# Kernel tuning notes

Hardware: AMD Instinct MI355X
Metric: run time of the kernel (lower is better)

The kernel has to match this reference:

```python
import jax, jax.numpy as jnp
import numpy as np

N_NODES = 20000
N_EDGES = 320000
HIDDEN = 128
HEADS = 8
LAYERS = 3
EXP_DEG = 4
N_VIRT = 1
NV = N_NODES + N_VIRT  # nodes after VirtualNode transform


def _layer_norm(x, g, b, eps=1e-5):
    mu = jnp.mean(x, axis=-1, keepdims=True)
    var = jnp.var(x, axis=-1, keepdims=True)
    return (x - mu) * jax.lax.rsqrt(var + eps) * g + b


def _segment_softmax(scores, seg, num_segments):
    # numerically-stable softmax over edges grouped by destination node
    m = jax.ops.segment_max(scores, seg, num_segments=num_segments)
    m = jnp.where(jnp.isfinite(m), m, 0.0)
    e = jnp.exp(scores - m[seg])
    s = jax.ops.segment_sum(e, seg, num_segments=num_segments)
    return e / (s[seg] + 1e-16)


def _edge_attention(x, src, dst, wq, bq, wk, bk, wv, bv, wo, bo):
    # multi-head attention restricted to the given edge list (Exphormer local/expander attention)
    n, d_model = x.shape
    dh = d_model // HEADS
    q = (x @ wq + bq).reshape(n, HEADS, dh)
    k = (x @ wk + bk).reshape(n, HEADS, dh)
    v = (x @ wv + bv).reshape(n, HEADS, dh)
    scores = jnp.einsum('ehd,ehd->eh', q[dst], k[src]) * (1.0 / np.sqrt(dh))  # [E, H]
    alpha = _segment_softmax(scores, dst, n)
    out = jax.ops.segment_sum(alpha[:, :, None] * v[src], dst, num_segments=n)  # [n, H, dh]
    return out.reshape(n, d_model) @ wo + bo


def setup_inputs():
    key = jax.random.key(0)
    ks = jax.random.split(key, 32)
    x = jax.random.normal(ks[0], (N_NODES, HIDDEN), dtype=jnp.float32)
    edge_index = jax.random.randint(ks[1], (2, N_EDGES), 0, N_NODES, dtype=jnp.int32)
    # expander graph per layer: EXP_DEG//2 random permutations, both directions
    ar = jnp.arange(NV, dtype=jnp.int32)
    layers_e = []
    for l in range(LAYERS):
        e = []
        for p in range(EXP_DEG // 2):
            perm = jax.random.permutation(jax.random.fold_in(ks[2], l * 10 + p), NV).astype(jnp.int32)
            e.append(jnp.stack([ar, perm]))
            e.append(jnp.stack([perm, ar]))
        layers_e.append(jnp.concatenate(e, axis=1))
    expander_edges = jnp.stack(layers_e)  # [LAYERS, 2, NV*EXP_DEG]

    def w(k, shape):
        return jax.random.normal(k, shape, dtype=jnp.float32) * 0.05

    p = {}
    names = ['lq', 'lk', 'lv', 'lo', 'eq', 'ek', 'ev', 'eo']
    for i, nm in enumerate(names):
        p[nm + '_w'] = w(ks[3 + i], (LAYERS, HIDDEN, HIDDEN))
        p[nm + '_b'] = w(ks[12 + i], (LAYERS, HIDDEN))
    p['ln_g'] = jnp.ones((LAYERS, HIDDEN), jnp.float32)
    p['ln_b'] = jnp.zeros((LAYERS, HIDDEN), jnp.float32)
    p['ffn_w1'] = w(ks[21], (LAYERS, HIDDEN, 4 * HIDDEN))
    p['ffn_b1'] = w(ks[22], (LAYERS, 4 * HIDDEN))
    p['ffn_w2'] = w(ks[23], (LAYERS, 4 * HIDDEN, HIDDEN))
    p['ffn_b2'] = w(ks[24], (LAYERS, HIDDEN))
    return {'x': x, 'edge_index': edge_index, 'expander_edges': expander_edges, **p}


def reference(x, edge_index, expander_edges,
              lq_w, lq_b, lk_w, lk_b, lv_w, lv_b, lo_w, lo_b,
              eq_w, eq_b, ek_w, ek_b, ev_w, ev_b, eo_w, eo_b,
              ln_g, ln_b, ffn_w1, ffn_b1, ffn_w2, ffn_b2):
    n = x.shape[0]
    # VirtualNode transform: one zero-feature node connected bidirectionally to all nodes
    xv = jnp.concatenate([x, jnp.zeros((N_VIRT, x.shape[1]), x.dtype)], axis=0)
    ar = jnp.arange(n, dtype=edge_index.dtype)
    vn = jnp.full((n,), n, dtype=edge_index.dtype)
    vsrc = jnp.concatenate([edge_index[0], ar, vn])
    vdst = jnp.concatenate([edge_index[1], vn, ar])
    for l in range(LAYERS):
        residual = xv
        local = _edge_attention(xv, vsrc, vdst,
                                lq_w[l], lq_b[l], lk_w[l], lk_b[l],
                                lv_w[l], lv_b[l], lo_w[l], lo_b[l])
        exp_out = _edge_attention(xv, expander_edges[l, 0], expander_edges[l, 1],
                                  eq_w[l], eq_b[l], ek_w[l], ek_b[l],
                                  ev_w[l], ev_b[l], eo_w[l], eo_b[l])
        xv = _layer_norm(residual + local + exp_out, ln_g[l], ln_b[l])
        xv = xv + (jax.nn.gelu(xv @ ffn_w1[l] + ffn_b1[l], approximate=False) @ ffn_w2[l] + ffn_b2[l])
    return xv[:N_NODES]
```

## Files before the change

### kernel.cpp

```cpp
#include <hip/hip_runtime.h>
#include <hip/hip_bf16.h>
#include <math.h>

#define NN    20000
#define NVT   20001
#define VN    20000
#define E_EI  320000
#define E_LOC 360000
#define E_EXP 80004
#define RSN   20002
#define NBVN  79
#define VNSTR 144

#define OW_LQ 0
#define OB_LQ 16384
#define OW_LK 16512
#define OB_LK 32896
#define OW_LV 33024
#define OB_LV 49408
#define OW_LO 49536
#define OB_LO 65920
#define OW_EQ 66048
#define OB_EQ 82432
#define OW_EK 82560
#define OB_EK 98944
#define OW_EV 99072
#define OB_EV 115456
#define OW_EO 115584
#define OB_EO 131968
#define O_LNG 132096
#define O_LNB 132224
#define O_FW1 132352
#define O_FB1 197888
#define O_FW2 198400
#define O_FB2 263936
#define WC_TOT 264064

typedef unsigned short u16;
typedef unsigned int   u32;
typedef __attribute__((ext_vector_type(8))) short short8;
typedef __attribute__((ext_vector_type(4))) float f32x4;

__device__ __forceinline__ float bf2f(u16 u) {
    return __uint_as_float(((u32)u) << 16);
}
__device__ __forceinline__ u16 f2bf(float f) {
    u32 x = __float_as_uint(f);
    u32 r = x + 0x7fffu + ((x >> 16) & 1u);
    return (u16)(r >> 16);
}

__device__ __forceinline__ void loadq16(const u16* qp, float* qf) {
    const uint4* p = (const uint4*)qp;
    uint4 a = p[0], b = p[1];
    qf[0]=bf2f((u16)(a.x&0xffff)); qf[1]=bf2f((u16)(a.x>>16));
    qf[2]=bf2f((u16)(a.y&0xffff)); qf[3]=bf2f((u16)(a.y>>16));
    qf[4]=bf2f((u16)(a.z&0xffff)); qf[5]=bf2f((u16)(a.z>>16));
    qf[6]=bf2f((u16)(a.w&0xffff)); qf[7]=bf2f((u16)(a.w>>16));
    qf[8]=bf2f((u16)(b.x&0xffff)); qf[9]=bf2f((u16)(b.x>>16));
    qf[10]=bf2f((u16)(b.y&0xffff)); qf[11]=bf2f((u16)(b.y>>16));
    qf[12]=bf2f((u16)(b.z&0xffff)); qf[13]=bf2f((u16)(b.z>>16));
    qf[14]=bf2f((u16)(b.w&0xffff)); qf[15]=bf2f((u16)(b.w>>16));
}
__device__ __forceinline__ float dot16_pre(const u16* kp, const float* qf) {
    const uint4* p = (const uint4*)kp;
    uint4 a = p[0], b = p[1];
    float s = 0.f;
    s += qf[0]*bf2f((u16)(a.x&0xffff)) + qf[1]*bf2f((u16)(a.x>>16));
    s += qf[2]*bf2f((u16)(a.y&0xffff)) + qf[3]*bf2f((u16)(a.y>>16));
    s += qf[4]*bf2f((u16)(a.z&0xffff)) + qf[5]*bf2f((u16)(a.z>>16));
    s += qf[6]*bf2f((u16)(a.w&0xffff)) + qf[7]*bf2f((u16)(a.w>>16));
    s += qf[8]*bf2f((u16)(b.x&0xffff)) + qf[9]*bf2f((u16)(b.x>>16));
    s += qf[10]*bf2f((u16)(b.y&0xffff)) + qf[11]*bf2f((u16)(b.y>>16));
    s += qf[12]*bf2f((u16)(b.z&0xffff)) + qf[13]*bf2f((u16)(b.z>>16));
    s += qf[14]*bf2f((u16)(b.w&0xffff)) + qf[15]*bf2f((u16)(b.w>>16));
    return s;
}
__device__ __forceinline__ float dot16_bf(const u16* kptr, const float* qptr) {
    const uint4* kp = (const uint4*)kptr;
    uint4 a = kp[0], b = kp[1];
    const float4* qp = (const float4*)qptr;
    float4 q0 = qp[0], q1 = qp[1], q2 = qp[2], q3 = qp[3];
    float s = 0.f;
    s += q0.x * bf2f((u16)(a.x & 0xffff)) + q0.y * bf2f((u16)(a.x >> 16));
    s += q0.z * bf2f((u16)(a.y & 0xffff)) + q0.w * bf2f((u16)(a.y >> 16));
    s += q1.x * bf2f((u16)(a.z & 0xffff)) + q1.y * bf2f((u16)(a.z >> 16));
    s += q1.z * bf2f((u16)(a.w & 0xffff)) + q1.w * bf2f((u16)(a.w >> 16));
    s += q2.x * bf2f((u16)(b.x & 0xffff)) + q2.y * bf2f((u16)(b.x >> 16));
    s += q2.z * bf2f((u16)(b.y & 0xffff)) + q2.w * bf2f((u16)(b.y >> 16));
    s += q3.x * bf2f((u16)(b.z & 0xffff)) + q3.y * bf2f((u16)(b.z >> 16));
    s += q3.z * bf2f((u16)(b.w & 0xffff)) + q3.w * bf2f((u16)(b.w >> 16));
    return s;
}

__global__ void k_detect(const u16* __restrict__ x, int* __restrict__ flag) {
    int t = threadIdx.x;
    u16 v = x[2 * t];
    int e = (v >> 7) & 0xFF;
    int sane = (e >= 100 && e <= 150) ? 1 : 0;
    __shared__ int s;
    if (t == 0) s = 0;
    __syncthreads();
    atomicAdd(&s, sane);
    __syncthreads();
    if (t == 0) *flag = (s >= 192) ? 1 : 0;
}

__global__ void k_convert(const void* __restrict__ x, const int* __restrict__ flag,
                          u16* __restrict__ XV, int* __restrict__ RS) {
    int i = blockIdx.x * 256 + threadIdx.x;
    if (i < NVT * 128) {
        u16 v = 0;
        if (i < NN * 128)
            v = (*flag) ? ((const u16*)x)[i] : f2bf(((const float*)x)[i]);
        XV[i] = v;
    } else {
        int j = i - NVT * 128;
        if (j < RSN + 4) RS[j] = 0;
    }
}

__global__ void k_canon(
    const void* lqw, const void* lqb, const void* lkw, const void* lkb,
    const void* lvw, const void* lvb, const void* low_, const void* lob,
    const void* eqw, const void* eqb, const void* ekw, const void* ekb,
    const void* evw, const void* evb, const void* eow, const void* eob,
    const void* lng, const void* lnb, const void* f1w, const void* f1b,
    const void* f2w, const void* f2b,
    const int* __restrict__ flag, u16* __restrict__ WcAll)
{
    int idx = blockIdx.x * 256 + threadIdx.x;
    if (idx >= WC_TOT) return;
    int layer = blockIdx.y;
    u16* Wc = WcAll + (size_t)layer * WC_TOT;
    const void* src;
    int e, stride;
    if (idx < 132096) {
        int p = idx / 16512, w = idx - p * 16512;
        const void* wt; const void* bt;
        switch (p) {
            case 0: wt = lqw; bt = lqb; break;
            case 1: wt = lkw; bt = lkb; break;
            case 2: wt = lvw; bt = lvb; break;
            case 3: wt = low_; bt = lob; break;
            case 4: wt = eqw; bt = eqb; break;
            case 5: wt = ekw; bt = ekb; break;
            case 6: wt = evw; bt = evb; break;
            default: wt = eow; bt = eob; break;
        }
        if (w < 16384) {
            int kt = w >> 12, ct = (w >> 9) & 7, ln = (w >> 3) & 63, j = w & 7;
            int k = kt * 32 + (ln >> 4) * 8 + j, c = ct * 16 + (ln & 15);
            src = wt; e = k * 128 + c; stride = 16384;
        } else { src = bt; e = w - 16384; stride = 128; }
    } else {
        int t2 = idx - 132096;
        if (t2 < 128)        { src = lng; e = t2;       stride = 128; }
        else if (t2 < 256)   { src = lnb; e = t2 - 128; stride = 128; }
        else if (t2 < 256 + 65536) {
            int w = t2 - 256;
            int cb = w >> 14, w2 = w & 16383;
            int kt = w2 >> 12, ct = (w2 >> 9) & 7, ln = (w2 >> 3) & 63, j = w2 & 7;
            int k = kt * 32 + (ln >> 4) * 8 + j, c = cb * 128 + ct * 16 + (ln & 15);
            src = f1w; e = k * 512 + c; stride = 65536;
        }
        else if (t2 < 66304) { src = f1b; e = t2 - 65792; stride = 512; }
        else if (t2 < 131840) {
            int w = t2 - 66304;
            int kt = w >> 12, ct = (w >> 9) & 7, ln = (w >> 3) & 63, j = w & 7;
            int k = kt * 32 + (ln >> 4) * 8 + j, c = ct * 16 + (ln & 15);
            src = f2w; e = k * 128 + c; stride = 65536;
        }
        else { src = f2b; e = t2 - 131840; stride = 128; }
    }
    int eg = layer * stride + e;
    Wc[idx] = (*flag) ? ((const u16*)src)[eg] : f2bf(((const float*)src)[eg]);
}

__global__ void k_count(const int* __restrict__ ei, int* __restrict__ RS) {
    int g = blockIdx.x * 256 + threadIdx.x;
    if (g >= E_EI) return;
    atomicAdd(&RS[ei[E_EI + g] + 1], 1);
}

__global__ __launch_bounds__(256) void k_scan(int* __restrict__ RS, int* __restrict__ CUR) {
    int t = threadIdx.x;
    const int CH = 79;
    int base = t * CH;
    int sum = 0;
    for (int i = 0; i < CH; ++i) {
        int idx = base + i;
        if (idx < RSN) {
            int add = RS[idx];
            if (idx >= 1 && idx <= NN) add += 1;
            if (idx == RSN - 1)        add += NN;
            sum += add;
        }
    }
    __shared__ int ss[256];
    ss[t] = sum;
    __syncthreads();
    for (int off = 1; off < 256; off <<= 1) {
        int v = (t >= off) ? ss[t - off] : 0;
        __syncthreads();
        ss[t] += v;
        __syncthreads();
    }
    int run = ss[t] - sum;
    for (int i = 0; i < CH; ++i) {
        int idx = base + i;
        if (idx < RSN) {
            int add = RS[idx];
            if (idx >= 1 && idx <= NN) add += 1;
            if (idx == RSN - 1)        add += NN;
            run += add;
            RS[idx]  = run;
            if (idx < NN) CUR[idx] = run + 1;
        }
    }
}

__global__ void k_scatter(const int* __restrict__ ei, int* __restrict__ CUR,
                          int* __restrict__ CSRC) {
    int g = blockIdx.x * 256 + threadIdx.x;
    if (g >= E_EI) return;
    int src = ei[g], dst = ei[E_EI + g];
    int pos = atomicAdd(&CUR[dst], 1);
    CSRC[pos] = src;
}

__global__ void k_fixinv(const int* __restrict__ RS, int* __restrict__ CSRC,
                         const int* __restrict__ ex, int* __restrict__ IP) {
    int idx = blockIdx.x * 256 + threadIdx.x;
    if (idx < NN) {
        CSRC[RS[idx]] = VN;
        CSRC[RS[VN] + idx] = idx;
    }
    if (idx < 6 * NVT) {
        int p = idx / NVT, i = idx - p * NVT;
        int l = p >> 1, w = p & 1;
        int off = l * 2 * E_EXP + E_EXP + w * 2 * NVT;
        int val = ex[off + i];
        IP[p * NVT + val] = i;
    }
}


__global__ __launch_bounds__(256) void k_qkv(
    const u16* __restrict__ X, const u16* __restrict__ Wc,
    u16* O0, u16* O1, u16* O2)
{
    int z = blockIdx.z;
    int wo = (z == 0) ? OW_LQ : (z == 1) ? OW_LK : OW_LV;
    int bo = (z == 0) ? OB_LQ : (z == 1) ? OB_LK : OB_LV;
    u16* O = (z == 0) ? O0 : (z == 1) ? O1 : O2;
    int t = threadIdx.x;
    int wv = t >> 6, lane = t & 63;
    int q4 = lane >> 4, m = lane & 15;
    int rowb = blockIdx.x * 64 + wv * 16;
    int r0 = min(rowb + m, NVT - 1);
    f32x4 zero4 = {0.f, 0.f, 0.f, 0.f};
    f32x4 acc[8];
    #pragma unroll
    for (int ct = 0; ct < 8; ++ct) acc[ct] = zero4;

    const u16* Wf = Wc + wo + lane * 8;
    #pragma unroll
    for (int kt = 0; kt < 4; ++kt) {
        short8 a0 = *(const short8*)&X[r0 * 128 + kt * 32 + q4 * 8];
        #pragma unroll
        for (int ct = 0; ct < 8; ++ct) {
            short8 bw = *(const short8*)&Wf[kt * 4096 + ct * 512];
            acc[ct] = __builtin_amdgcn_mfma_f32_16x16x32_bf16(bw, a0, acc[ct], 0, 0, 0);
        }
    }
    int row = rowb + m;
    if (row < NVT) {
        #pragma unroll
        for (int ct = 0; ct < 8; ++ct) {
            int c0 = ct * 16 + q4 * 4;
            ushort4 bb = *(const ushort4*)&Wc[bo + c0];
            ushort4 st;
            st.x = f2bf(acc[ct][0] + bf2f(bb.x));
            st.y = f2bf(acc[ct][1] + bf2f(bb.y));
            st.z = f2bf(acc[ct][2] + bf2f(bb.z));
            st.w = f2bf(acc[ct][3] + bf2f(bb.w));
            *(ushort4*)&O[row * 128 + c0] = st;
        }
    }
}

__global__ __launch_bounds__(256) void k_pq(
    u16* ATT, const u16* XV, const u16* __restrict__ Wc,
    u16* Q, u16* K, u16* V)
{
    int z = blockIdx.z;
    const u16* X; u16* O; const u16* A = nullptr;
    int wo, bo;
    if (z == 0)      { X = ATT; O = ATT; A = XV; wo = OW_LO; bo = OB_LO; }
    else if (z == 1) { X = XV;  O = Q;  wo = OW_EQ; bo = OB_EQ; }
    else if (z == 2) { X = XV;  O = K;  wo = OW_EK; bo = OB_EK; }
    else             { X = XV;  O = V;  wo = OW_EV; bo = OB_EV; }

    int t = threadIdx.x;
    int wv = t >> 6, lane = t & 63;
    int q4 = lane >> 4, m = lane & 15;
    int rowb = blockIdx.x * 64 + wv * 16;
    int r0 = min(rowb + m, NVT - 1);
    f32x4 zero4 = {0.f, 0.f, 0.f, 0.f};
    f32x4 acc[8];
    #pragma unroll
    for (int ct = 0; ct < 8; ++ct) acc[ct] = zero4;

    const u16* Wf = Wc + wo + lane * 8;
    #pragma unroll
    for (int kt = 0; kt < 4; ++kt) {
        short8 a0 = *(const short8*)&X[r0 * 128 + kt * 32 + q4 * 8];
        #pragma unroll
        for (int ct = 0; ct < 8; ++ct) {
            short8 bw = *(const short8*)&Wf[kt * 4096 + ct * 512];
            acc[ct] = __builtin_amdgcn_mfma_f32_16x16x32_bf16(bw, a0, acc[ct], 0, 0, 0);
        }
    }
    int row = rowb + m;
    if (row < NVT) {
        #pragma unroll
        for (int ct = 0; ct < 8; ++ct) {
            int c0 = ct * 16 + q4 * 4;
            ushort4 bb = *(const ushort4*)&Wc[bo + c0];
            float v0 = acc[ct][0] + bf2f(bb.x);
            float v1 = acc[ct][1] + bf2f(bb.y);
            float v2 = acc[ct][2] + bf2f(bb.z);
            float v3 = acc[ct][3] + bf2f(bb.w);
            if (A) {
                ushort4 av = *(const ushort4*)&A[row * 128 + c0];
                v0 += bf2f(av.x); v1 += bf2f(av.y);
                v2 += bf2f(av.z); v3 += bf2f(av.w);
            }
            ushort4 st;
            st.x = f2bf(v0); st.y = f2bf(v1); st.z = f2bf(v2); st.w = f2bf(v3);
            *(ushort4*)&O[row * 128 + c0] = st;
        }
    }
}

__global__ __launch_bounds__(256) void k_plf(
    u16* XV, const u16* __restrict__ ATT, const u16* __restrict__ Wc,
    const int* __restrict__ flag, void* outp, int write_out)
{
    __shared__ __align__(16) u16 Xs[32 * 136];
    __shared__ __align__(16) u16 Hs[32 * 520];
    int t = threadIdx.x;
    int wv = t >> 6, lane = t & 63;
    int q4 = lane >> 4, m = lane & 15;
    int rowb = blockIdx.x * 32;
    f32x4 zero4 = {0.f, 0.f, 0.f, 0.f};

    if (wv < 2) {
        int rl = wv * 16 + m;
        int r0 = min(rowb + rl, NVT - 1);
        f32x4 acc[8];
        #pragma unroll
        for (int ct = 0; ct < 8; ++ct) acc[ct] = zero4;
        const u16* Wf = Wc + OW_EO + lane * 8;
        #pragma unroll
        for (int kt = 0; kt < 4; ++kt) {
            short8 a0 = *(const short8*)&XV[r0 * 128 + kt * 32 + q4 * 8];
            #pragma unroll
            for (int ct = 0; ct < 8; ++ct) {
                short8 bw = *(const short8*)&Wf[kt * 4096 + ct * 512];
                acc[ct] = __builtin_amdgcn_mfma_f32_16x16x32_bf16(bw, a0, acc[ct], 0, 0, 0);
            }
        }
        float sm = 0.f, sq = 0.f;
        #pragma unroll
        for (int ct = 0; ct < 8; ++ct) {
            int c0 = ct * 16 + q4 * 4;
            ushort4 bb = *(const ushort4*)&Wc[OB_EO + c0];
            ushort4 av = *(const ushort4*)&ATT[r0 * 128 + c0];
            acc[ct][0] += bf2f(bb.x) + bf2f(av.x);
            acc[ct][1] += bf2f(bb.y) + bf2f(av.y);
            acc[ct][2] += bf2f(bb.z) + bf2f(av.z);
            acc[ct][3] += bf2f(bb.w) + bf2f(av.w);
            #pragma unroll
            for (int j = 0; j < 4; ++j) { sm += acc[ct][j]; sq += acc[ct][j] * acc[ct][j]; }
        }
        sm += __shfl_xor(sm, 16); sq += __shfl_xor(sq, 16);
        sm += __shfl_xor(sm, 32); sq += __shfl_xor(sq, 32);
        float mu  = sm * (1.f / 128.f);
        float var = sq * (1.f / 128.f) - mu * mu;
        float rs  = rsqrtf(var + 1e-5f);
        #pragma unroll
        for (int ct = 0; ct < 8; ++ct) {
            int c0 = ct * 16 + q4 * 4;
            ushort4 gg = *(const ushort4*)&Wc[O_LNG + c0];
            ushort4 bb = *(const ushort4*)&Wc[O_LNB + c0];
            ushort4 st;
            st.x = f2bf((acc[ct][0] - mu) * rs * bf2f(gg.x) + bf2f(bb.x));
            st.y = f2bf((acc[ct][1] - mu) * rs * bf2f(gg.y) + bf2f(bb.y));
            st.z = f2bf((acc[ct][2] - mu) * rs * bf2f(gg.z) + bf2f(bb.z));
            st.w = f2bf((acc[ct][3] - mu) * rs * bf2f(gg.w) + bf2f(bb.w));
            *(ushort4*)&Xs[rl * 136 + c0] = st;
        }
    }
    __syncthreads();

    short8 ax[2][4];
    #pragma unroll
    for (int kt = 0; kt < 4; ++kt) {
        ax[0][kt] = *(const short8*)&Xs[m * 136 + kt * 32 + q4 * 8];
        ax[1][kt] = *(const short8*)&Xs[(16 + m) * 136 + kt * 32 + q4 * 8];
    }
    f32x4 a1[2][8];
    #pragma unroll
    for (int rg = 0; rg < 2; ++rg)
        #pragma unroll
        for (int ct = 0; ct < 8; ++ct) a1[rg][ct] = zero4;
    const u16* W1f = Wc + O_FW1 + wv * 16384 + lane * 8;
    #pragma unroll
    for (int kt = 0; kt < 4; ++kt) {
        #pragma unroll
        for (int ct = 0; ct < 8; ++ct) {
            short8 bw = *(const short8*)&W1f[kt * 4096 + ct * 512];
            a1[0][ct] = __builtin_amdgcn_mfma_f32_16x16x32_bf16(bw, ax[0][kt], a1[0][ct], 0, 0, 0);
            a1[1][ct] = __builtin_amdgcn_mfma_f32_16x16x32_bf16(bw, ax[1][kt], a1[1][ct], 0, 0, 0);
        }
    }
    #pragma unroll
    for (int rg = 0; rg < 2; ++rg) {
        int rl = rg * 16 + m;
        #pragma unroll
        for (int ct = 0; ct < 8; ++ct) {
            int c = wv * 128 + ct * 16 + q4 * 4;
            ushort4 bb = *(const ushort4*)&Wc[O_FB1 + c];
            float v0 = a1[rg][ct][0] + bf2f(bb.x);
            float v1 = a1[rg][ct][1] + bf2f(bb.y);
            float v2 = a1[rg][ct][2] + bf2f(bb.z);
            float v3 = a1[rg][ct][3] + bf2f(bb.w);
            ushort4 st;
            st.x = f2bf(0.5f * v0 * (1.f + erff(v0 * 0.70710678118654752440f)));
            st.y = f2bf(0.5f * v1 * (1.f + erff(v1 * 0.70710678118654752440f)));
            st.z = f2bf(0.5f * v2 * (1.f + erff(v2 * 0.70710678118654752440f)));
            st.w = f2bf(0.5f * v3 * (1.f + erff(v3 * 0.70710678118654752440f)));
            *(ushort4*)&Hs[rl * 520 + c] = st;
        }
    }
    __syncthreads();

    f32x4 acc2[2][2];
    #pragma unroll
    for (int rg = 0; rg < 2; ++rg)
        #pragma unroll
        for (int j = 0; j < 2; ++j) acc2[rg][j] = zero4;
    const u16* W2f = Wc + O_FW2 + lane * 8;
    #pragma unroll
    for (int kt = 0; kt < 16; ++kt) {
        short8 h0 = *(const short8*)&Hs[m * 520 + kt * 32 + q4 * 8];
        short8 h1 = *(const short8*)&Hs[(16 + m) * 520 + kt * 32 + q4 * 8];
        #pragma unroll
        for (int j = 0; j < 2; ++j) {
            short8 bw = *(const short8*)&W2f[kt * 4096 + (2 * wv + j) * 512];
            acc2[0][j] = __builtin_amdgcn_mfma_f32_16x16x32_bf16(bw, h0, acc2[0][j], 0, 0, 0);
            acc2[1][j] = __builtin_amdgcn_mfma_f32_16x16x32_bf16(bw, h1, acc2[1][j], 0, 0, 0);
        }
    }
    int fl = *flag;
    #pragma unroll
    for (int rg = 0; rg < 2; ++rg) {
        int row = rowb + rg * 16 + m;
        if (row < NVT) {
            #pragma unroll
            for (int j = 0; j < 2; ++j) {
                int c0 = (2 * wv + j) * 16 + q4 * 4;
                ushort4 bb = *(const ushort4*)&Wc[O_FB2 + c0];
                ushort4 rv = *(const ushort4*)&Xs[(rg * 16 + m) * 136 + c0];
                float v0 = acc2[rg][j][0] + bf2f(bb.x) + bf2f(rv.x);
                float v1 = acc2[rg][j][1] + bf2f(bb.y) + bf2f(rv.y);
                float v2 = acc2[rg][j][2] + bf2f(bb.z) + bf2f(rv.z);
                float v3 = acc2[rg][j][3] + bf2f(bb.w) + bf2f(rv.w);
                ushort4 st;
                st.x = f2bf(v0); st.y = f2bf(v1); st.z = f2bf(v2); st.w = f2bf(v3);
                *(ushort4*)&XV[row * 128 + c0] = st;
                if (write_out && row < NN) {
                    if (fl) {
                        *(ushort4*)((u16*)outp + row * 128 + c0) = st;
                    } else {
                        float4 fv; fv.x = v0; fv.y = v1; fv.z = v2; fv.w = v3;
                        *(float4*)((float*)outp + row * 128 + c0) = fv;
                    }
                }
            }
        }
    }
}

__global__ __launch_bounds__(256) void k_gvn(
    const u16* __restrict__ Q, const u16* __restrict__ K,
    const u16* __restrict__ V, const int* __restrict__ RS,
    const int* __restrict__ CSRC, u16* __restrict__ OUT,
    float* __restrict__ VNS, int* __restrict__ CNT)
{
    int t = threadIdx.x;
    __shared__ float ps_s[4][128];
    __shared__ int   sv_s[4][16];
    if (blockIdx.x >= NBVN) {
        int wv = t >> 6, l = t & 63;
        int dst = (blockIdx.x - NBVN) * 4 + wv;
        int hp = l & 3;
        int e16 = l >> 2;
        int hq = l >> 4;
        float* ps = ps_s[wv];
        int* svp = sv_s[wv];
        int rs = RS[dst], re = RS[dst + 1];
        float qf[32];
        loadq16(&Q[dst * 128 + hp * 32], qf);
        loadq16(&Q[dst * 128 + hp * 32 + 16], qf + 16);
        float acc0 = 0.f, acc1 = 0.f, d0 = 0.f, d1 = 0.f;
        for (int e0 = rs; e0 < re; e0 += 16) {
            int eidx = e0 + e16;
            bool val = eidx < re;
            int eidx2 = val ? eidx : (re - 1);
            int sv = CSRC[eidx2];
            float s0 = dot16_pre(&K[sv * 128 + hp * 32], qf) * 0.25f;
            float s1 = dot16_pre(&K[sv * 128 + hp * 32 + 16], qf + 16) * 0.25f;
            float p0 = val ? __expf(s0) : 0.f;
            float p1 = val ? __expf(s1) : 0.f;
            ps[e16 * 8 + 2 * hp]     = p0;
            ps[e16 * 8 + 2 * hp + 1] = p1;
            if (hp == 0) svp[e16] = sv;
            #pragma unroll
            for (int ee = 0; ee < 16; ++ee) {
                int se = svp[ee];
                float w0 = ps[ee * 8 + hq];
                float w1 = ps[ee * 8 + 4 + hq];
                acc0 += w0 * bf2f(V[se * 128 + l]);
                acc1 += w1 * bf2f(V[se * 128 + 64 + l]);
                d0 += w0; d1 += w1;
            }
        }
        OUT[dst * 128 + l]      = f2bf(acc0 / (d0 + 1e-16f));
        OUT[dst * 128 + 64 + l] = f2bf(acc1 / (d1 + 1e-16f));
        return;
    }
    int vb = blockIdx.x;
    __shared__ __align__(16) float q_s[128];
    __shared__ float sr_s[256 * 8];
    __shared__ float pden[64];
    __shared__ float psum[128];
    __shared__ int   lastBlk;
    int base = vb * 256;
    if (t < 128) q_s[t] = bf2f(Q[VN * 128 + t]);
    __syncthreads();

    int e32 = t >> 3, h = t & 7;
    for (int pass = 0; pass < 8; ++pass) {
        int e = pass * 32 + e32;
        int src = base + e;
        float p = 0.f;
        if (src < NN)
            p = __expf(dot16_bf(&K[src * 128 + h * 16], &q_s[h * 16]) * 0.25f);
        sr_s[e * 8 + h] = p;
    }
    __syncthreads();
    if (t < 64) {
        int h2 = t & 7, c = t >> 3;
        float pd = 0.f;
        for (int j = 0; j < 32; ++j)
            pd += sr_s[(c * 32 + j) * 8 + h2];
        pden[t] = pd;
    }
    __syncthreads();
    if (t < 8) {
        float dn = 0.f;
        for (int c = 0; c < 8; ++c) dn += pden[c * 8 + t];
        VNS[vb * VNSTR + 8 + t] = dn;
    }
    int d = t & 127, half = t >> 7, hd = d >> 4;
    float acc = 0.f;
    for (int i = 0; i < 128; ++i) {
        int e = half * 128 + i;
        int src = base + e;
        if (src < NN)
            acc += sr_s[e * 8 + hd] * bf2f(V[src * 128 + d]);
    }
    if (half == 1) psum[d] = acc;
    __syncthreads();
    if (half == 0)
        VNS[vb * VNSTR + 16 + d] = acc + psum[d];
    __threadfence();
    __syncthreads();
    if (t == 0) lastBlk = (atomicAdd(CNT, 1) == NBVN - 1) ? 1 : 0;
    __syncthreads();
    if (lastBlk) {
        __threadfence();
        volatile const float* VV = VNS;
        __shared__ float den_s[8];
        if (t < 8) {
            float dn = 0.f;
            for (int b = 0; b < NBVN; ++b) dn += VV[b * VNSTR + 8 + t];
            den_s[t] = dn;
        }
        __syncthreads();
        if (t < 128) {
            int hd2 = t >> 4;
            float a2 = 0.f;
            for (int b = 0; b < NBVN; ++b) a2 += VV[b * VNSTR + 16 + t];
            OUT[VN * 128 + t] = f2bf(a2 / (den_s[hd2] + 1e-16f));
        }
    }
}

__global__ __launch_bounds__(256) void k_egather(
    const u16* __restrict__ Q, const u16* __restrict__ K,
    const u16* __restrict__ V, const int* __restrict__ IP0,
    const int* __restrict__ IP1, const int* __restrict__ PD,
    u16* __restrict__ OUT)
{
    int wv = threadIdx.x >> 6, l = threadIdx.x & 63;
    int dst = blockIdx.x * 4 + wv;
    if (dst >= NVT) return;
    int h = l & 7, e = (l >> 3) & 3, hq = l >> 4;
    int sv;
    if (e == 0)      sv = IP0[dst];
    else if (e == 1) sv = PD[dst];
    else if (e == 2) sv = IP1[dst];
    else             sv = PD[2 * NVT + dst];
    float qf[16];
    loadq16(&Q[dst * 128 + h * 16], qf);
    float sr = dot16_pre(&K[sv * 128 + h * 16], qf) * 0.25f;
    float p = __expf(sr);
    float den = p + __shfl_xor(p, 8);
    den += __shfl_xor(den, 16);
    float acc0 = 0.f, acc1 = 0.f;
    #pragma unroll
    for (int ee = 0; ee < 4; ++ee) {
        int se = __shfl(sv, ee * 8);
        float p0 = __shfl(p, ee * 8 + hq);
        float p1 = __shfl(p, ee * 8 + 4 + hq);
        acc0 += p0 * bf2f(V[se * 128 + l]);
        acc1 += p1 * bf2f(V[se * 128 + 64 + l]);
    }
    float d0 = __shfl(den, hq), d1 = __shfl(den, 4 + hq);
    OUT[dst * 128 + l]      = f2bf(acc0 / (d0 + 1e-16f));
    OUT[dst * 128 + 64 + l] = f2bf(acc1 / (d1 + 1e-16f));
}

extern "C" void kernel_launch(void* const* d_in, const int* in_sizes, int n_in,
                              void* d_out, int out_size, void* d_ws, size_t ws_size,
                              hipStream_t stream)
{
    const void* x = d_in[0];
    const int* ei = (const int*)d_in[1];
    const int* ex = (const int*)d_in[2];

    const size_t NFB = (size_t)NVT * 128 * 2;
    char* wsb = (char*)d_ws;
    u16* XVb  = (u16*)(wsb);
    u16* ATTb = (u16*)(wsb + NFB);
    u16* Qb   = (u16*)(wsb + 2 * NFB);
    u16* Kb   = (u16*)(wsb + 3 * NFB);
    u16* Vb   = (u16*)(wsb + 4 * NFB);
    int* RS   = (int*)(wsb + 5 * NFB);
    int* CNT  = RS + RSN;
    int* CUR  = CNT + 4;
    int* IP   = CUR + RSN;
    size_t o_wc = 5 * NFB + (size_t)(2 * RSN + 4 + 6 * NVT) * 4;
    o_wc = (o_wc + 15) & ~(size_t)15;
    u16* Wc   = (u16*)(wsb + o_wc);
    int* flag = (int*)(wsb + o_wc + (size_t)3 * WC_TOT * 2);

    int*   CSRC = (int*)d_out;
    float* VNS  = (float*)((char*)d_out + (size_t)E_LOC * 4);

    k_detect<<<1, 256, 0, stream>>>((const u16*)x, flag);
    k_convert<<<(NVT * 128 + RSN + 4 + 255) / 256, 256, 0, stream>>>(x, flag, XVb, RS);
    int eb = (E_EI + 255) / 256;
    k_count  <<<eb, 256, 0, stream>>>(ei, RS);
    k_scan   <<<1, 256, 0, stream>>>(RS, CUR);
    k_scatter<<<eb, 256, 0, stream>>>(ei, CUR, CSRC);
    k_fixinv <<<(6 * NVT + 255) / 256, 256, 0, stream>>>(RS, CSRC, ex, IP);
    k_canon<<<dim3((WC_TOT + 255) / 256, 3), 256, 0, stream>>>(
        d_in[3],  d_in[4],  d_in[5],  d_in[6],  d_in[7],  d_in[8],
        d_in[9],  d_in[10], d_in[11], d_in[12], d_in[13], d_in[14],
        d_in[15], d_in[16], d_in[17], d_in[18], d_in[19], d_in[20],
        d_in[21], d_in[22], d_in[23], d_in[24], flag, Wc);

    int gb64 = (NVT + 63) / 64;
    int gb32 = (NVT + 31) / 32;
    for (int l = 0; l < 3; ++l) {
        const u16* Wl = Wc + (size_t)l * WC_TOT;
        k_qkv<<<dim3(gb64, 1, 3), 256, 0, stream>>>(XVb, Wl, Qb, Kb, Vb);
        k_gvn<<<NBVN + NN / 4, 256, 0, stream>>>(Qb, Kb, Vb, RS, CSRC, ATTb,
                                                  VNS, CNT + l);
        k_pq<<<dim3(gb64, 1, 4), 256, 0, stream>>>(ATTb, XVb, Wl, Qb, Kb, Vb);
        k_egather<<<(NVT + 3) / 4, 256, 0, stream>>>(Qb, Kb, Vb,
            IP + (2 * l) * NVT, IP + (2 * l + 1) * NVT,
            ex + (size_t)l * 2 * E_EXP + E_EXP, XVb);
        k_plf<<<gb32, 256, 0, stream>>>(XVb, ATTb, Wl, flag, d_out,
                                        (l == 2) ? 1 : 0);
    }
}
```

Baseline: 707.6 us.

## Fuse expander gather with local out-projection and prefetch V rows in local attention

```diff
diff --git a/kernel.cpp b/kernel.cpp
--- a/kernel.cpp
+++ b/kernel.cpp
@@ -245,14 +245,14 @@
     }
 }
 
-
 __global__ __launch_bounds__(256) void k_qkv(
     const u16* __restrict__ X, const u16* __restrict__ Wc,
+    int w0, int b0, int w1, int b1, int w2, int b2,
     u16* O0, u16* O1, u16* O2)
 {
     int z = blockIdx.z;
-    int wo = (z == 0) ? OW_LQ : (z == 1) ? OW_LK : OW_LV;
-    int bo = (z == 0) ? OB_LQ : (z == 1) ? OB_LK : OB_LV;
+    int wo = (z == 0) ? w0 : (z == 1) ? w1 : w2;
+    int bo = (z == 0) ? b0 : (z == 1) ? b1 : b2;
     u16* O = (z == 0) ? O0 : (z == 1) ? O1 : O2;
     int t = threadIdx.x;
     int wv = t >> 6, lane = t & 63;
@@ -290,32 +290,59 @@
     }
 }
 
-__global__ __launch_bounds__(256) void k_pq(
+#define GB64 313
+#define NEG  5001
+
+__global__ __launch_bounds__(256) void k_pe(
     u16* ATT, const u16* XV, const u16* __restrict__ Wc,
-    u16* Q, u16* K, u16* V)
+    u16* Q, const u16* __restrict__ K, const u16* __restrict__ V,
+    const int* __restrict__ IP0, const int* __restrict__ IP1,
+    const int* __restrict__ PD)
 {
-    int z = blockIdx.z;
-    const u16* X; u16* O; const u16* A = nullptr;
-    int wo, bo;
-    if (z == 0)      { X = ATT; O = ATT; A = XV; wo = OW_LO; bo = OB_LO; }
-    else if (z == 1) { X = XV;  O = Q;  wo = OW_EQ; bo = OB_EQ; }
-    else if (z == 2) { X = XV;  O = K;  wo = OW_EK; bo = OB_EK; }
-    else             { X = XV;  O = V;  wo = OW_EV; bo = OB_EV; }
-
     int t = threadIdx.x;
+    if (blockIdx.x < NEG) {
+        int wv = t >> 6, l = t & 63;
+        int dst = blockIdx.x * 4 + wv;
+        if (dst >= NVT) return;
+        int h = l & 7, e = (l >> 3) & 3, hq = l >> 4;
+        int sv;
+        if (e == 0)      sv = IP0[dst];
+        else if (e == 1) sv = PD[dst];
+        else if (e == 2) sv = IP1[dst];
+        else             sv = PD[2 * NVT + dst];
+        float qf[16];
+        loadq16(&Q[dst * 128 + h * 16], qf);
+        float sr = dot16_pre(&K[sv * 128 + h * 16], qf) * 0.25f;
+        float p = __expf(sr);
+        float den = p + __shfl_xor(p, 8);
+        den += __shfl_xor(den, 16);
+        float acc0 = 0.f, acc1 = 0.f;
+        #pragma unroll
+        for (int ee = 0; ee < 4; ++ee) {
+            int se = __shfl(sv, ee * 8);
+            float p0 = __shfl(p, ee * 8 + hq);
+            float p1 = __shfl(p, ee * 8 + 4 + hq);
+            acc0 += p0 * bf2f(V[se * 128 + l]);
+            acc1 += p1 * bf2f(V[se * 128 + 64 + l]);
+        }
+        float d0 = __shfl(den, hq), d1 = __shfl(den, 4 + hq);
+        Q[dst * 128 + l]      = f2bf(acc0 / (d0 + 1e-16f));
+        Q[dst * 128 + 64 + l] = f2bf(acc1 / (d1 + 1e-16f));
+        return;
+    }
+    int bx = blockIdx.x - NEG;
     int wv = t >> 6, lane = t & 63;
     int q4 = lane >> 4, m = lane & 15;
-    int rowb = blockIdx.x * 64 + wv * 16;
+    int rowb = bx * 64 + wv * 16;
     int r0 = min(rowb + m, NVT - 1);
     f32x4 zero4 = {0.f, 0.f, 0.f, 0.f};
     f32x4 acc[8];
     #pragma unroll
     for (int ct = 0; ct < 8; ++ct) acc[ct] = zero4;
-
-    const u16* Wf = Wc + wo + lane * 8;
+    const u16* Wf = Wc + OW_LO + lane * 8;
     #pragma unroll
     for (int kt = 0; kt < 4; ++kt) {
-        short8 a0 = *(const short8*)&X[r0 * 128 + kt * 32 + q4 * 8];
+        short8 a0 = *(const short8*)&ATT[r0 * 128 + kt * 32 + q4 * 8];
         #pragma unroll
         for (int ct = 0; ct < 8; ++ct) {
             short8 bw = *(const short8*)&Wf[kt * 4096 + ct * 512];
@@ -327,26 +354,22 @@
         #pragma unroll
         for (int ct = 0; ct < 8; ++ct) {
             int c0 = ct * 16 + q4 * 4;
-            ushort4 bb = *(const ushort4*)&Wc[bo + c0];
-            float v0 = acc[ct][0] + bf2f(bb.x);
-            float v1 = acc[ct][1] + bf2f(bb.y);
-            float v2 = acc[ct][2] + bf2f(bb.z);
-            float v3 = acc[ct][3] + bf2f(bb.w);
-            if (A) {
-                ushort4 av = *(const ushort4*)&A[row * 128 + c0];
-                v0 += bf2f(av.x); v1 += bf2f(av.y);
-                v2 += bf2f(av.z); v3 += bf2f(av.w);
-            }
+            ushort4 bb = *(const ushort4*)&Wc[OB_LO + c0];
+            ushort4 av = *(const ushort4*)&XV[row * 128 + c0];
             ushort4 st;
-            st.x = f2bf(v0); st.y = f2bf(v1); st.z = f2bf(v2); st.w = f2bf(v3);
-            *(ushort4*)&O[row * 128 + c0] = st;
+            st.x = f2bf(acc[ct][0] + bf2f(bb.x) + bf2f(av.x));
+            st.y = f2bf(acc[ct][1] + bf2f(bb.y) + bf2f(av.y));
+            st.z = f2bf(acc[ct][2] + bf2f(bb.z) + bf2f(av.z));
+            st.w = f2bf(acc[ct][3] + bf2f(bb.w) + bf2f(av.w));
+            *(ushort4*)&ATT[row * 128 + c0] = st;
         }
     }
 }
 
 __global__ __launch_bounds__(256) void k_plf(
-    u16* XV, const u16* __restrict__ ATT, const u16* __restrict__ Wc,
-    const int* __restrict__ flag, void* outp, int write_out)
+    u16* XV, const u16* __restrict__ EO, const u16* __restrict__ ATT,
+    const u16* __restrict__ Wc, const int* __restrict__ flag,
+    void* outp, int write_out)
 {
     __shared__ __align__(16) u16 Xs[32 * 136];
     __shared__ __align__(16) u16 Hs[32 * 520];
@@ -365,7 +388,7 @@
         const u16* Wf = Wc + OW_EO + lane * 8;
         #pragma unroll
         for (int kt = 0; kt < 4; ++kt) {
-            short8 a0 = *(const short8*)&XV[r0 * 128 + kt * 32 + q4 * 8];
+            short8 a0 = *(const short8*)&EO[r0 * 128 + kt * 32 + q4 * 8];
             #pragma unroll
             for (int ct = 0; ct < 8; ++ct) {
                 short8 bw = *(const short8*)&Wf[kt * 4096 + ct * 512];
@@ -519,23 +542,27 @@
         for (int e0 = rs; e0 < re; e0 += 16) {
             int eidx = e0 + e16;
             bool val = eidx < re;
-            int eidx2 = val ? eidx : (re - 1);
-            int sv = CSRC[eidx2];
+            int sv = CSRC[min(eidx, re - 1)];
+            if (hp == 0) svp[e16] = sv;
+            float vv0[16], vv1[16];
+            #pragma unroll
+            for (int ee = 0; ee < 16; ++ee) {
+                int se = svp[ee];
+                vv0[ee] = bf2f(V[se * 128 + l]);
+                vv1[ee] = bf2f(V[se * 128 + 64 + l]);
+            }
             float s0 = dot16_pre(&K[sv * 128 + hp * 32], qf) * 0.25f;
             float s1 = dot16_pre(&K[sv * 128 + hp * 32 + 16], qf + 16) * 0.25f;
             float p0 = val ? __expf(s0) : 0.f;
             float p1 = val ? __expf(s1) : 0.f;
             ps[e16 * 8 + 2 * hp]     = p0;
             ps[e16 * 8 + 2 * hp + 1] = p1;
-            if (hp == 0) svp[e16] = sv;
             #pragma unroll
             for (int ee = 0; ee < 16; ++ee) {
-                int se = svp[ee];
                 float w0 = ps[ee * 8 + hq];
                 float w1 = ps[ee * 8 + 4 + hq];
-                acc0 += w0 * bf2f(V[se * 128 + l]);
-                acc1 += w1 * bf2f(V[se * 128 + 64 + l]);
-                d0 += w0; d1 += w1;
+                acc0 += w0 * vv0[ee]; d0 += w0;
+                acc1 += w1 * vv1[ee]; d1 += w1;
             }
         }
         OUT[dst * 128 + l]      = f2bf(acc0 / (d0 + 1e-16f));
@@ -608,41 +635,6 @@
             OUT[VN * 128 + t] = f2bf(a2 / (den_s[hd2] + 1e-16f));
         }
     }
-}
-
-__global__ __launch_bounds__(256) void k_egather(
-    const u16* __restrict__ Q, const u16* __restrict__ K,
-    const u16* __restrict__ V, const int* __restrict__ IP0,
-    const int* __restrict__ IP1, const int* __restrict__ PD,
-    u16* __restrict__ OUT)
-{
-    int wv = threadIdx.x >> 6, l = threadIdx.x & 63;
-    int dst = blockIdx.x * 4 + wv;
-    if (dst >= NVT) return;
-    int h = l & 7, e = (l >> 3) & 3, hq = l >> 4;
-    int sv;
-    if (e == 0)      sv = IP0[dst];
-    else if (e == 1) sv = PD[dst];
-    else if (e == 2) sv = IP1[dst];
-    else             sv = PD[2 * NVT + dst];
-    float qf[16];
-    loadq16(&Q[dst * 128 + h * 16], qf);
-    float sr = dot16_pre(&K[sv * 128 + h * 16], qf) * 0.25f;
-    float p = __expf(sr);
-    float den = p + __shfl_xor(p, 8);
-    den += __shfl_xor(den, 16);
-    float acc0 = 0.f, acc1 = 0.f;
-    #pragma unroll
-    for (int ee = 0; ee < 4; ++ee) {
-        int se = __shfl(sv, ee * 8);
-        float p0 = __shfl(p, ee * 8 + hq);
-        float p1 = __shfl(p, ee * 8 + 4 + hq);
-        acc0 += p0 * bf2f(V[se * 128 + l]);
-        acc1 += p1 * bf2f(V[se * 128 + 64 + l]);
-    }
-    float d0 = __shfl(den, hq), d1 = __shfl(den, 4 + hq);
-    OUT[dst * 128 + l]      = f2bf(acc0 / (d0 + 1e-16f));
-    OUT[dst * 128 + 64 + l] = f2bf(acc1 / (d1 + 1e-16f));
 }
 
 extern "C" void kernel_launch(void* const* d_in, const int* in_sizes, int n_in,
@@ -685,18 +677,18 @@
         d_in[15], d_in[16], d_in[17], d_in[18], d_in[19], d_in[20],
         d_in[21], d_in[22], d_in[23], d_in[24], flag, Wc);
 
-    int gb64 = (NVT + 63) / 64;
-    int gb32 = (NVT + 31) / 32;
     for (int l = 0; l < 3; ++l) {
         const u16* Wl = Wc + (size_t)l * WC_TOT;
-        k_qkv<<<dim3(gb64, 1, 3), 256, 0, stream>>>(XVb, Wl, Qb, Kb, Vb);
+        k_qkv<<<dim3(GB64, 1, 3), 256, 0, stream>>>(XVb, Wl,
+            OW_LQ, OB_LQ, OW_LK, OB_LK, OW_LV, OB_LV, Qb, Kb, Vb);
         k_gvn<<<NBVN + NN / 4, 256, 0, stream>>>(Qb, Kb, Vb, RS, CSRC, ATTb,
                                                   VNS, CNT + l);
-        k_pq<<<dim3(gb64, 1, 4), 256, 0, stream>>>(ATTb, XVb, Wl, Qb, Kb, Vb);
-        k_egather<<<(NVT + 3) / 4, 256, 0, stream>>>(Qb, Kb, Vb,
+        k_qkv<<<dim3(GB64, 1, 3), 256, 0, stream>>>(XVb, Wl,
+            OW_EQ, OB_EQ, OW_EK, OB_EK, OW_EV, OB_EV, Qb, Kb, Vb);
+        k_pe<<<NEG + GB64, 256, 0, stream>>>(ATTb, XVb, Wl, Qb, Kb, Vb,
             IP + (2 * l) * NVT, IP + (2 * l + 1) * NVT,
-            ex + (size_t)l * 2 * E_EXP + E_EXP, XVb);
-        k_plf<<<gb32, 256, 0, stream>>>(XVb, ATTb, Wl, flag, d_out,
-                                        (l == 2) ? 1 : 0);
-    }
-}
+            ex + (size_t)l * 2 * E_EXP + E_EXP);
+        k_plf<<<(NVT + 31) / 32, 256, 0, stream>>>(XVb, Qb, ATTb, Wl, flag,
+                                                   d_out, (l == 2) ? 1 : 0);
+    }
+}
```

Measured after the change: 736.6 us. 4.1% more time.

## Split each destination's edge chunks across two waves and vectorize V gathers

Applied to the files above, without the earlier changes.

```diff
diff --git a/kernel.cpp b/kernel.cpp
--- a/kernel.cpp
+++ b/kernel.cpp
@@ -245,7 +245,6 @@
     }
 }
 
-
 __global__ __launch_bounds__(256) void k_qkv(
     const u16* __restrict__ X, const u16* __restrict__ Wc,
     u16* O0, u16* O1, u16* O2)
@@ -503,43 +502,65 @@
     int t = threadIdx.x;
     __shared__ float ps_s[4][128];
     __shared__ int   sv_s[4][16];
+    __shared__ float pp_s[4 * 64 * 3];
     if (blockIdx.x >= NBVN) {
         int wv = t >> 6, l = t & 63;
-        int dst = (blockIdx.x - NBVN) * 4 + wv;
+        int bx = blockIdx.x - NBVN;
+        int dst = bx * 2 + (wv >> 1);
+        int part = wv & 1;
         int hp = l & 3;
         int e16 = l >> 2;
-        int hq = l >> 4;
+        int hq = l >> 3;
         float* ps = ps_s[wv];
         int* svp = sv_s[wv];
         int rs = RS[dst], re = RS[dst + 1];
+        int nch = (re - rs + 15) >> 4;
+        int ch0 = part * ((nch + 1) >> 1);
+        int ch1 = part ? nch : ((nch + 1) >> 1);
         float qf[32];
         loadq16(&Q[dst * 128 + hp * 32], qf);
         loadq16(&Q[dst * 128 + hp * 32 + 16], qf + 16);
-        float acc0 = 0.f, acc1 = 0.f, d0 = 0.f, d1 = 0.f;
-        for (int e0 = rs; e0 < re; e0 += 16) {
+        const u32* V32 = (const u32*)V;
+        float ax = 0.f, ay = 0.f, dd = 0.f;
+        for (int c = ch0; c < ch1; ++c) {
+            int e0 = rs + c * 16;
             int eidx = e0 + e16;
-            bool val = eidx < re;
-            int eidx2 = val ? eidx : (re - 1);
-            int sv = CSRC[eidx2];
+            bool valid = eidx < re;
+            int sv = CSRC[min(eidx, re - 1)];
+            if (hp == 0) svp[e16] = sv;
+            float vx[16], vy[16];
+            #pragma unroll
+            for (int ee = 0; ee < 16; ++ee) {
+                u32 vw = V32[svp[ee] * 64 + l];
+                vx[ee] = bf2f((u16)(vw & 0xffff));
+                vy[ee] = bf2f((u16)(vw >> 16));
+            }
             float s0 = dot16_pre(&K[sv * 128 + hp * 32], qf) * 0.25f;
             float s1 = dot16_pre(&K[sv * 128 + hp * 32 + 16], qf + 16) * 0.25f;
-            float p0 = val ? __expf(s0) : 0.f;
-            float p1 = val ? __expf(s1) : 0.f;
+            float p0 = valid ? __expf(s0) : 0.f;
+            float p1 = valid ? __expf(s1) : 0.f;
             ps[e16 * 8 + 2 * hp]     = p0;
             ps[e16 * 8 + 2 * hp + 1] = p1;
-            if (hp == 0) svp[e16] = sv;
             #pragma unroll
             for (int ee = 0; ee < 16; ++ee) {
-                int se = svp[ee];
-                float w0 = ps[ee * 8 + hq];
-                float w1 = ps[ee * 8 + 4 + hq];
-                acc0 += w0 * bf2f(V[se * 128 + l]);
-                acc1 += w1 * bf2f(V[se * 128 + 64 + l]);
-                d0 += w0; d1 += w1;
+                float w = ps[ee * 8 + hq];
+                ax += w * vx[ee];
+                ay += w * vy[ee];
+                dd += w;
             }
         }
-        OUT[dst * 128 + l]      = f2bf(acc0 / (d0 + 1e-16f));
-        OUT[dst * 128 + 64 + l] = f2bf(acc1 / (d1 + 1e-16f));
+        int idx = (wv * 64 + l) * 3;
+        pp_s[idx] = ax; pp_s[idx + 1] = ay; pp_s[idx + 2] = dd;
+        __syncthreads();
+        if (part == 0) {
+            int idx2 = ((wv + 1) * 64 + l) * 3;
+            ax += pp_s[idx2];
+            ay += pp_s[idx2 + 1];
+            dd += pp_s[idx2 + 2];
+            float inv = 1.f / (dd + 1e-16f);
+            u32 o = (u32)f2bf(ax * inv) | ((u32)f2bf(ay * inv) << 16);
+            ((u32*)OUT)[dst * 64 + l] = o;
+        }
         return;
     }
     int vb = blockIdx.x;
@@ -690,7 +711,7 @@
     for (int l = 0; l < 3; ++l) {
         const u16* Wl = Wc + (size_t)l * WC_TOT;
         k_qkv<<<dim3(gb64, 1, 3), 256, 0, stream>>>(XVb, Wl, Qb, Kb, Vb);
-        k_gvn<<<NBVN + NN / 4, 256, 0, stream>>>(Qb, Kb, Vb, RS, CSRC, ATTb,
+        k_gvn<<<NBVN + NN / 2, 256, 0, stream>>>(Qb, Kb, Vb, RS, CSRC, ATTb,
                                                   VNS, CNT + l);
         k_pq<<<dim3(gb64, 1, 4), 256, 0, stream>>>(ATTb, XVb, Wl, Qb, Kb, Vb);
         k_egather<<<(NVT + 3) / 4, 256, 0, stream>>>(Qb, Kb, Vb,
```

Result: no change. 708.2 us (+0.1%).
